# Optimization experiments

Measured on AMD Instinct MI355X. Metric: run time of the kernel, lower is better.

Reference implementation:

```python
import jax, jax.numpy as jnp
import numpy as np

B, IN_CS = 2, 32
H = W = D = 96

def conv1x1(w, v):
    # 1x1x1 Conv3d without bias: per-voxel matvec over channels
    return jnp.einsum('oc,bcxyz->boxyz', w, v)

def kron(a, b):
    # per-voxel outer product over channels; index order i*c2+j matches torch view
    bs, c1 = a.shape[:2]
    c2 = b.shape[1]
    out = jnp.einsum('bixyz,bjxyz->bijxyz', a, b)
    return out.reshape(bs, c1 * c2, *a.shape[2:])

def setup_inputs() -> dict:
    key = jax.random.key(0)
    ks = jax.random.split(key, 7)
    s = 0.1  # weight init scale
    return {
        'x': jax.random.normal(ks[0], (B, IN_CS, H, W, D), jnp.float32),
        'd_all': jax.random.normal(ks[1], (B, 6, H, W, D), jnp.float32),
        'W1': jax.random.normal(ks[2], (16, 2), jnp.float32) * s,
        'W2': jax.random.normal(ks[3], (3, 16), jnp.float32) * s,
        'G1': jax.random.normal(ks[4], (IN_CS, 27), jnp.float32) * s,
        'G2': jax.random.normal(ks[5], (2 * IN_CS, IN_CS), jnp.float32) * s,
        'G3': jax.random.normal(ks[6], (IN_CS, 2 * IN_CS), jnp.float32) * s,
    }

def reference(x, d_all, W1, W2, G1, G2, G3):
    def encode(v):
        return conv1x1(W2, jax.nn.relu(conv1x1(W1, v)))
    x_x = encode(d_all[:, 0:2])
    y_y = encode(d_all[:, 2:4])
    z_z = encode(d_all[:, 4:6])
    enced = kron(kron(x_x, y_y), z_z)  # [B, 27, H, W, D]
    h = jax.nn.relu(conv1x1(G1, enced))
    h = jax.nn.relu(conv1x1(G2, h))
    filters = conv1x1(G3, h)  # [B, IN_CS, H, W, D]
    return jnp.sum(x * filters, axis=1, keepdims=True)
```

## Files before the change

### kernel.cpp

```cpp
#include <hip/hip_runtime.h>


typedef _Float16 f16x8 __attribute__((ext_vector_type(8)));
typedef _Float16 f16x4 __attribute__((ext_vector_type(4)));
typedef float    f32x4 __attribute__((ext_vector_type(4)));

constexpr int V3   = 96 * 96 * 96;
constexpr int NVOX = 2 * V3;
constexpr int TV   = 256;
constexpr int NBLK = NVOX / TV;
constexpr int S    = 72;
constexpr int SD   = 36;

constexpr float SCALE     = 16384.f;
constexpr float INV_SCALE = 1.f / 16384.f;

constexpr int N_TILES  = 10;
constexpr int WS_BYTES = N_TILES * 64 * 8 * 2;

#define LDS_FENCE() asm volatile("s_waitcnt lgkmcnt(0)" ::: "memory")

__device__ __forceinline__ f16x8 build_frag(int tile, int n16, int quad,
                                            const float* __restrict__ G1,
                                            const float* __restrict__ G2,
                                            const float* __restrict__ G3) {
    f16x8 v;
    const int k0 = quad * 8;
#pragma unroll
    for (int j = 0; j < 8; ++j) {
        float f = 0.f;
        const int k = k0 + j;
        if (tile < 2) {
            if (k < 27) f = G1[(tile * 16 + n16) * 27 + k];
        } else if (tile < 6) {
            f = G2[((tile - 2) * 16 + n16) * 32 + k];
        } else {
            const int kh = (tile - 6) >> 1, nh = (tile - 6) & 1;
            f = G3[(nh * 16 + n16) * 64 + kh * 32 + k];
        }
        v[j] = (_Float16)f;
    }
    return v;
}

__global__ __launch_bounds__(256) void pack_weights(
    const float* __restrict__ G1, const float* __restrict__ G2,
    const float* __restrict__ G3, _Float16* __restrict__ wf)
{
    for (int slot = threadIdx.x; slot < N_TILES * 64; slot += 256) {
        const int tile = slot >> 6;
        const int lane = slot & 63;
        const f16x8 v = build_frag(tile, lane & 15, lane >> 4, G1, G2, G3);
        *(f16x8*)&wf[slot * 8] = v;
    }
}

template <bool USE_WS>
__global__ __launch_bounds__(256) void metaclf_mfma3(
    const float* __restrict__ x,
    const float* __restrict__ d_all,
    const float* __restrict__ W1,
    const float* __restrict__ W2,
    const float* __restrict__ G1,
    const float* __restrict__ G2,
    const float* __restrict__ G3,
    const _Float16* __restrict__ wf,
    float* __restrict__ out)
{
    __shared__ _Float16 lds[TV * S];
    float* const ldsf = (float*)lds;

    const int t    = threadIdx.x;
    const int lane = t & 63;
    const int wave = t >> 6;
    const int n16  = lane & 15;
    const int quad = lane >> 4;
    const int g0   = wave * 4;

    const int gidx = blockIdx.x * TV + t;
    const int b = (gidx >= V3) ? 1 : 0;
    const int v = gidx - b * V3;

    auto frag = [&](int tile) -> f16x8 {
        if constexpr (USE_WS) return *(const f16x8*)&wf[(tile * 64 + lane) * 8];
        else                  return build_frag(tile, n16, quad, G1, G2, G3);
    };

    {
        float e[3][3];
#pragma unroll
        for (int a = 0; a < 3; ++a) {
            const float d0 = d_all[(b * 6 + 2 * a    ) * V3 + v];
            const float d1 = d_all[(b * 6 + 2 * a + 1) * V3 + v];
            float a0 = 0.f, a1 = 0.f, a2 = 0.f;
#pragma unroll
            for (int k = 0; k < 16; ++k) {
                const float tt = fmaxf(fmaf(W1[k * 2], d0, W1[k * 2 + 1] * d1), 0.f);
                a0 = fmaf(W2[0 * 16 + k], tt, a0);
                a1 = fmaf(W2[1 * 16 + k], tt, a1);
                a2 = fmaf(W2[2 * 16 + k], tt, a2);
            }
            e[a][0] = a0; e[a][1] = a1; e[a][2] = a2;
        }
        _Float16 row[32];
#pragma unroll
        for (int i = 0; i < 3; ++i)
#pragma unroll
            for (int j = 0; j < 3; ++j) {
                const float p = e[0][i] * e[1][j] * SCALE;
#pragma unroll
                for (int k = 0; k < 3; ++k)
                    row[i * 9 + j * 3 + k] = (_Float16)(p * e[2][k]);
            }
#pragma unroll
        for (int m = 27; m < 32; ++m) row[m] = (_Float16)0.f;

        f16x8* dst = (f16x8*)&lds[t * S];
#pragma unroll
        for (int i = 0; i < 4; ++i) dst[i] = ((const f16x8*)row)[i];
    }
    LDS_FENCE();

    {
        const f16x8 b0 = frag(0);
        const f16x8 b1 = frag(1);
#pragma unroll
        for (int g = 0; g < 4; ++g) {
            const int rowv = (g0 + g) * 16;
            const f16x8 a = *(const f16x8*)&lds[(rowv + n16) * S + quad * 8];
            f32x4 c0 = {0.f, 0.f, 0.f, 0.f}, c1 = {0.f, 0.f, 0.f, 0.f};
            c0 = __builtin_amdgcn_mfma_f32_16x16x32_f16(b0, a, c0, 0, 0, 0);
            c1 = __builtin_amdgcn_mfma_f32_16x16x32_f16(b1, a, c1, 0, 0, 0);
            f16x4 h0, h1;
#pragma unroll
            for (int r = 0; r < 4; ++r) {
                h0[r] = (_Float16)fmaxf(c0[r], 0.f);
                h1[r] = (_Float16)fmaxf(c1[r], 0.f);
            }
            *(f16x4*)&lds[(rowv + n16) * S + quad * 4]      = h0;
            *(f16x4*)&lds[(rowv + n16) * S + 16 + quad * 4] = h1;
        }
    }
    LDS_FENCE();

    {
        f16x8 w[4];
#pragma unroll
        for (int q = 0; q < 4; ++q) w[q] = frag(2 + q);
#pragma unroll
        for (int g = 0; g < 4; ++g) {
            const int rowv = (g0 + g) * 16;
            const f16x8 a = *(const f16x8*)&lds[(rowv + n16) * S + quad * 8];
            f32x4 c[4];
#pragma unroll
            for (int q = 0; q < 4; ++q) {
                c[q] = (f32x4){0.f, 0.f, 0.f, 0.f};
                c[q] = __builtin_amdgcn_mfma_f32_16x16x32_f16(w[q], a, c[q], 0, 0, 0);
            }
#pragma unroll
            for (int q = 0; q < 4; ++q) {
                f16x4 h;
#pragma unroll
                for (int r = 0; r < 4; ++r) h[r] = (_Float16)fmaxf(c[q][r], 0.f);
                *(f16x4*)&lds[(rowv + n16) * S + q * 16 + quad * 4] = h;
            }
        }
    }
    LDS_FENCE();

    {
        const f16x8 w00 = frag(6), w01 = frag(7), w10 = frag(8), w11 = frag(9);
#pragma unroll
        for (int g = 0; g < 4; ++g) {
            const int rowv = (g0 + g) * 16;
            const f16x8 a0 = *(const f16x8*)&lds[(rowv + n16) * S + quad * 8];
            const f16x8 a1 = *(const f16x8*)&lds[(rowv + n16) * S + 32 + quad * 8];
            f32x4 c0 = {0.f, 0.f, 0.f, 0.f}, c1 = {0.f, 0.f, 0.f, 0.f};
            c0 = __builtin_amdgcn_mfma_f32_16x16x32_f16(w00, a0, c0, 0, 0, 0);
            c0 = __builtin_amdgcn_mfma_f32_16x16x32_f16(w10, a1, c0, 0, 0, 0);
            c1 = __builtin_amdgcn_mfma_f32_16x16x32_f16(w01, a0, c1, 0, 0, 0);
            c1 = __builtin_amdgcn_mfma_f32_16x16x32_f16(w11, a1, c1, 0, 0, 0);
            *(f32x4*)&ldsf[(rowv + n16) * SD + quad * 4]      = c0;
            *(f32x4*)&ldsf[(rowv + n16) * SD + 16 + quad * 4] = c1;
        }
    }
    LDS_FENCE();

    {
        const float* xb = x + (size_t)(b * 32) * V3 + v;
        float sum = 0.f;
#pragma unroll
        for (int i = 0; i < 8; ++i) {
            const f32x4 f = *(const f32x4*)&ldsf[t * SD + i * 4];
#pragma unroll
            for (int r = 0; r < 4; ++r)
                sum = fmaf(xb[(size_t)(i * 4 + r) * V3], f[r], sum);
        }
        out[b * V3 + v] = sum * INV_SCALE;
    }
}

extern "C" void kernel_launch(void* const* d_in, const int* in_sizes, int n_in,
                              void* d_out, int out_size, void* d_ws, size_t ws_size,
                              hipStream_t stream) {
    const float* x     = (const float*)d_in[0];
    const float* d_all = (const float*)d_in[1];
    const float* W1    = (const float*)d_in[2];
    const float* W2    = (const float*)d_in[3];
    const float* G1    = (const float*)d_in[4];
    const float* G2    = (const float*)d_in[5];
    const float* G3    = (const float*)d_in[6];
    float* out = (float*)d_out;

    if (ws_size >= (size_t)WS_BYTES) {
        _Float16* wf = (_Float16*)d_ws;
        pack_weights<<<1, 256, 0, stream>>>(G1, G2, G3, wf);
        metaclf_mfma3<true><<<NBLK, 256, 0, stream>>>(
            x, d_all, W1, W2, G1, G2, G3, wf, out);
    } else {
        metaclf_mfma3<false><<<NBLK, 256, 0, stream>>>(
            x, d_all, W1, W2, G1, G2, G3, nullptr, out);
    }
}
```

Measured before the change: 349.4 us.

## Chain MLP layers in registers via permuted weight rows, prefetch inputs early

Weight fragments are re-packed with a permuted output-channel order so that each MFMA accumulator layout directly forms the next layer's B operand. This lets the three conv layers chain in registers without LDS round-trips or fences between them. d_all, x and all ten weight fragments are loaded up front so global latency overlaps the encode stage. The final dot with x is done on the MFMA output layout with cross-lane shuffles, and launch bounds now request 4 blocks per CU. The cost is higher register pressure (32 x values plus 10 fragments held live), which the occupancy hint may not accommodate.

Result: no change. 348.5 us (median of 2 runs) (-0.3%).

```diff
diff --git a/kernel.cpp b/kernel.cpp
--- a/kernel.cpp
+++ b/kernel.cpp
@@ -10,7 +10,6 @@
 constexpr int TV   = 256;
 constexpr int NBLK = NVOX / TV;
 constexpr int S    = 72;
-constexpr int SD   = 36;
 
 constexpr float SCALE     = 16384.f;
 constexpr float INV_SCALE = 1.f / 16384.f;
@@ -18,25 +17,31 @@
 constexpr int N_TILES  = 10;
 constexpr int WS_BYTES = N_TILES * 64 * 8 * 2;
 
-#define LDS_FENCE() asm volatile("s_waitcnt lgkmcnt(0)" ::: "memory")
-
-__device__ __forceinline__ f16x8 build_frag(int tile, int n16, int quad,
+#define LDS_FENCE()  asm volatile("s_waitcnt lgkmcnt(0)" ::: "memory")
+#define ISSUE_FENCE() asm volatile("" ::: "memory")
+
+__device__ __forceinline__ f16x8 build_frag(int tile, int m_, int quad,
                                             const float* __restrict__ G1,
                                             const float* __restrict__ G2,
                                             const float* __restrict__ G3) {
     f16x8 v;
     const int k0 = quad * 8;
+    const int g8 = (m_ >> 2) * 8 + (m_ & 3);
 #pragma unroll
     for (int j = 0; j < 8; ++j) {
         float f = 0.f;
         const int k = k0 + j;
         if (tile < 2) {
-            if (k < 27) f = G1[(tile * 16 + n16) * 27 + k];
+            const int ch = g8 + tile * 4;
+            if (k < 27) f = G1[ch * 27 + k];
         } else if (tile < 6) {
-            f = G2[((tile - 2) * 16 + n16) * 32 + k];
+            const int T  = tile - 2;
+            const int ch = (T >> 1) * 32 + (T & 1) * 4 + g8;
+            f = G2[ch * 32 + k];
         } else {
-            const int kh = (tile - 6) >> 1, nh = (tile - 6) & 1;
-            f = G3[(nh * 16 + n16) * 64 + kh * 32 + k];
+            const int U  = tile - 6;
+            const int ch = g8 + (U & 1) * 4;
+            f = G3[ch * 64 + (U >> 1) * 32 + k];
         }
         v[j] = (_Float16)f;
     }
@@ -56,7 +61,7 @@
 }
 
 template <bool USE_WS>
-__global__ __launch_bounds__(256) void metaclf_mfma3(
+__global__ __launch_bounds__(256, 4) void metaclf_mfma4(
     const float* __restrict__ x,
     const float* __restrict__ d_all,
     const float* __restrict__ W1,
@@ -68,7 +73,6 @@
     float* __restrict__ out)
 {
     __shared__ _Float16 lds[TV * S];
-    float* const ldsf = (float*)lds;
 
     const int t    = threadIdx.x;
     const int lane = t & 63;
@@ -80,18 +84,40 @@
     const int gidx = blockIdx.x * TV + t;
     const int b = (gidx >= V3) ? 1 : 0;
     const int v = gidx - b * V3;
-
-    auto frag = [&](int tile) -> f16x8 {
-        if constexpr (USE_WS) return *(const f16x8*)&wf[(tile * 64 + lane) * 8];
-        else                  return build_frag(tile, n16, quad, G1, G2, G3);
-    };
+    const int vw = v - lane;
+
+    float dv[6];
+#pragma unroll
+    for (int i = 0; i < 6; ++i) dv[i] = d_all[(size_t)(b * 6 + i) * V3 + v];
+    ISSUE_FENCE();
+
+    f16x8 wfr[10];
+    if constexpr (USE_WS) {
+#pragma unroll
+        for (int i = 0; i < N_TILES; ++i)
+            wfr[i] = *(const f16x8*)&wf[(i * 64 + lane) * 8];
+    } else {
+#pragma unroll
+        for (int i = 0; i < N_TILES; ++i)
+            wfr[i] = build_frag(i, n16, quad, G1, G2, G3);
+    }
+    ISSUE_FENCE();
+
+    float xv[32];
+    {
+        const float* xb = x + ((size_t)(b * 32 + 8 * quad)) * V3 + (vw + n16);
+#pragma unroll
+        for (int g = 0; g < 4; ++g)
+#pragma unroll
+            for (int j = 0; j < 8; ++j)
+                xv[g * 8 + j] = xb[(size_t)j * V3 + g * 16];
+    }
 
     {
         float e[3][3];
 #pragma unroll
         for (int a = 0; a < 3; ++a) {
-            const float d0 = d_all[(b * 6 + 2 * a    ) * V3 + v];
-            const float d1 = d_all[(b * 6 + 2 * a + 1) * V3 + v];
+            const float d0 = dv[2 * a], d1 = dv[2 * a + 1];
             float a0 = 0.f, a1 = 0.f, a2 = 0.f;
 #pragma unroll
             for (int k = 0; k < 16; ++k) {
@@ -121,83 +147,55 @@
     }
     LDS_FENCE();
 
-    {
-        const f16x8 b0 = frag(0);
-        const f16x8 b1 = frag(1);
-#pragma unroll
-        for (int g = 0; g < 4; ++g) {
-            const int rowv = (g0 + g) * 16;
-            const f16x8 a = *(const f16x8*)&lds[(rowv + n16) * S + quad * 8];
-            f32x4 c0 = {0.f, 0.f, 0.f, 0.f}, c1 = {0.f, 0.f, 0.f, 0.f};
-            c0 = __builtin_amdgcn_mfma_f32_16x16x32_f16(b0, a, c0, 0, 0, 0);
-            c1 = __builtin_amdgcn_mfma_f32_16x16x32_f16(b1, a, c1, 0, 0, 0);
-            f16x4 h0, h1;
-#pragma unroll
-            for (int r = 0; r < 4; ++r) {
-                h0[r] = (_Float16)fmaxf(c0[r], 0.f);
-                h1[r] = (_Float16)fmaxf(c1[r], 0.f);
-            }
-            *(f16x4*)&lds[(rowv + n16) * S + quad * 4]      = h0;
-            *(f16x4*)&lds[(rowv + n16) * S + 16 + quad * 4] = h1;
-        }
-    }
-    LDS_FENCE();
-
-    {
-        f16x8 w[4];
-#pragma unroll
-        for (int q = 0; q < 4; ++q) w[q] = frag(2 + q);
-#pragma unroll
-        for (int g = 0; g < 4; ++g) {
-            const int rowv = (g0 + g) * 16;
-            const f16x8 a = *(const f16x8*)&lds[(rowv + n16) * S + quad * 8];
-            f32x4 c[4];
-#pragma unroll
-            for (int q = 0; q < 4; ++q) {
-                c[q] = (f32x4){0.f, 0.f, 0.f, 0.f};
-                c[q] = __builtin_amdgcn_mfma_f32_16x16x32_f16(w[q], a, c[q], 0, 0, 0);
-            }
-#pragma unroll
-            for (int q = 0; q < 4; ++q) {
-                f16x4 h;
-#pragma unroll
-                for (int r = 0; r < 4; ++r) h[r] = (_Float16)fmaxf(c[q][r], 0.f);
-                *(f16x4*)&lds[(rowv + n16) * S + q * 16 + quad * 4] = h;
-            }
-        }
-    }
-    LDS_FENCE();
-
-    {
-        const f16x8 w00 = frag(6), w01 = frag(7), w10 = frag(8), w11 = frag(9);
-#pragma unroll
-        for (int g = 0; g < 4; ++g) {
-            const int rowv = (g0 + g) * 16;
-            const f16x8 a0 = *(const f16x8*)&lds[(rowv + n16) * S + quad * 8];
-            const f16x8 a1 = *(const f16x8*)&lds[(rowv + n16) * S + 32 + quad * 8];
-            f32x4 c0 = {0.f, 0.f, 0.f, 0.f}, c1 = {0.f, 0.f, 0.f, 0.f};
-            c0 = __builtin_amdgcn_mfma_f32_16x16x32_f16(w00, a0, c0, 0, 0, 0);
-            c0 = __builtin_amdgcn_mfma_f32_16x16x32_f16(w10, a1, c0, 0, 0, 0);
-            c1 = __builtin_amdgcn_mfma_f32_16x16x32_f16(w01, a0, c1, 0, 0, 0);
-            c1 = __builtin_amdgcn_mfma_f32_16x16x32_f16(w11, a1, c1, 0, 0, 0);
-            *(f32x4*)&ldsf[(rowv + n16) * SD + quad * 4]      = c0;
-            *(f32x4*)&ldsf[(rowv + n16) * SD + 16 + quad * 4] = c1;
-        }
-    }
-    LDS_FENCE();
-
-    {
-        const float* xb = x + (size_t)(b * 32) * V3 + v;
-        float sum = 0.f;
-#pragma unroll
-        for (int i = 0; i < 8; ++i) {
-            const f32x4 f = *(const f32x4*)&ldsf[t * SD + i * 4];
-#pragma unroll
-            for (int r = 0; r < 4; ++r)
-                sum = fmaf(xb[(size_t)(i * 4 + r) * V3], f[r], sum);
-        }
-        out[b * V3 + v] = sum * INV_SCALE;
-    }
+    float res = 0.f;
+#pragma unroll
+    for (int g = 0; g < 4; ++g) {
+        const int rowv = (g0 + g) * 16;
+        const f16x8 ef = *(const f16x8*)&lds[(rowv + n16) * S + quad * 8];
+
+        f32x4 c0 = {0.f, 0.f, 0.f, 0.f}, c1 = {0.f, 0.f, 0.f, 0.f};
+        c0 = __builtin_amdgcn_mfma_f32_16x16x32_f16(wfr[0], ef, c0, 0, 0, 0);
+        c1 = __builtin_amdgcn_mfma_f32_16x16x32_f16(wfr[1], ef, c1, 0, 0, 0);
+        f16x8 b2;
+#pragma unroll
+        for (int r = 0; r < 4; ++r) {
+            b2[r]     = (_Float16)fmaxf(c0[r], 0.f);
+            b2[4 + r] = (_Float16)fmaxf(c1[r], 0.f);
+        }
+
+        f32x4 h[4];
+#pragma unroll
+        for (int q4 = 0; q4 < 4; ++q4) {
+            h[q4] = (f32x4){0.f, 0.f, 0.f, 0.f};
+            h[q4] = __builtin_amdgcn_mfma_f32_16x16x32_f16(wfr[2 + q4], b2, h[q4], 0, 0, 0);
+        }
+        f16x8 a0, a1;
+#pragma unroll
+        for (int r = 0; r < 4; ++r) {
+            a0[r]     = (_Float16)fmaxf(h[0][r], 0.f);
+            a0[4 + r] = (_Float16)fmaxf(h[1][r], 0.f);
+            a1[r]     = (_Float16)fmaxf(h[2][r], 0.f);
+            a1[4 + r] = (_Float16)fmaxf(h[3][r], 0.f);
+        }
+
+        f32x4 d0 = {0.f, 0.f, 0.f, 0.f}, d1 = {0.f, 0.f, 0.f, 0.f};
+        d0 = __builtin_amdgcn_mfma_f32_16x16x32_f16(wfr[6], a0, d0, 0, 0, 0);
+        d0 = __builtin_amdgcn_mfma_f32_16x16x32_f16(wfr[8], a1, d0, 0, 0, 0);
+        d1 = __builtin_amdgcn_mfma_f32_16x16x32_f16(wfr[7], a0, d1, 0, 0, 0);
+        d1 = __builtin_amdgcn_mfma_f32_16x16x32_f16(wfr[9], a1, d1, 0, 0, 0);
+
+        float p = 0.f;
+#pragma unroll
+        for (int r = 0; r < 4; ++r) {
+            p = fmaf(d0[r], xv[g * 8 + r],     p);
+            p = fmaf(d1[r], xv[g * 8 + 4 + r], p);
+        }
+        p += __shfl_xor(p, 16);
+        p += __shfl_xor(p, 32);
+        if (g == quad) res = p;
+    }
+
+    out[(size_t)b * V3 + v] = res * INV_SCALE;
 }
 
 extern "C" void kernel_launch(void* const* d_in, const int* in_sizes, int n_in,
@@ -215,10 +213,10 @@
     if (ws_size >= (size_t)WS_BYTES) {
         _Float16* wf = (_Float16*)d_ws;
         pack_weights<<<1, 256, 0, stream>>>(G1, G2, G3, wf);
-        metaclf_mfma3<true><<<NBLK, 256, 0, stream>>>(
+        metaclf_mfma4<true><<<NBLK, 256, 0, stream>>>(
             x, d_all, W1, W2, G1, G2, G3, wf, out);
     } else {
-        metaclf_mfma3<false><<<NBLK, 256, 0, stream>>>(
+        metaclf_mfma4<false><<<NBLK, 256, 0, stream>>>(
             x, d_all, W1, W2, G1, G2, G3, nullptr, out);
     }
 }
```
